# Optimization experiments

Measured on AMD Instinct MI355X. Metric: run time of the kernel, lower is better.

The kernel has to match this reference:

```python
import jax, jax.numpy as jnp
import numpy as np

B, S, HID, H = 2, 2048, 1024, 16
D_HEAD = HID // H  # 64
EPS = 1e-5


def _gammas():
    lo, hi = np.log(1.0 / 512.0), np.log(1.0 / 32.0)
    return (1.0 - np.exp(np.linspace(lo, hi, H))).astype(np.float32)


def _decay_mask():
    # D[h, n, m] = gamma_h^(n-m) for n >= m else 0  (causal exponential decay)
    gam = jnp.asarray(_gammas())                      # [H]
    pos = jnp.arange(S, dtype=jnp.float32)
    diff = pos[:, None] - pos[None, :]                # [S, S]
    keep = diff >= 0
    logg = jnp.log(gam)[:, None, None]                # [H,1,1]
    safe = jnp.where(keep, diff, 0.0)[None]           # avoid inf for masked entries
    return jnp.where(keep[None], jnp.exp(safe * logg), 0.0)  # [H, S, S]


def setup_inputs() -> dict:
    key = jax.random.key(0)
    ks = jax.random.split(key, 10)
    rn = lambda k, shape, s=1.0: jax.random.normal(k, shape, dtype=jnp.float32) * s
    return {
        "x": rn(ks[0], (B, S, HID)),
        "wq": rn(ks[1], (H, D_HEAD, D_HEAD), 1.0 / np.sqrt(D_HEAD)),
        "bq": rn(ks[2], (H, D_HEAD), 0.02),
        "wk": rn(ks[3], (H, D_HEAD, D_HEAD), 1.0 / np.sqrt(D_HEAD)),
        "bk": rn(ks[4], (H, D_HEAD), 0.02),
        "wv": rn(ks[5], (H, D_HEAD, D_HEAD), 1.0 / np.sqrt(D_HEAD)),
        "theta": rn(ks[6], (H, D_HEAD), 1.0 / D_HEAD),
        "gn_weight": jnp.ones((HID,), jnp.float32),
        "gn_bias": jnp.zeros((HID,), jnp.float32),
        "weight1": rn(ks[7], (HID, HID), 1.0 / HID),
        "weight2": rn(ks[8], (HID, HID), 1.0 / HID),
    }


def reference(x, wq, bq, wk, bk, wv, theta, gn_weight, gn_bias, weight1, weight2):
    # Per-head retention (all heads vectorized; torch loops over heads).
    xh = x.reshape(B, S, H, D_HEAD)
    q = jnp.einsum('bshd,hde->bshe', xh, wq) + bq
    k = jnp.einsum('bshd,hde->bshe', xh, wk) + bk
    v = jnp.einsum('bshd,hde->bshe', xh, wv)
    # Complex rotary factors exp(i*n*theta) on q, conj on k -> real part of q k^H:
    ang = jnp.arange(S, dtype=jnp.float32)[:, None, None] * theta[None]  # [S,H,d]
    cs, sn = jnp.cos(ang), jnp.sin(ang)
    scores = (jnp.einsum('bshd,bthd->bhst', q * cs, k * cs)
              + jnp.einsum('bshd,bthd->bhst', q * sn, k * sn))  # Re(QK^H) [B,H,S,S]
    scores = scores * _decay_mask()[None]                        # decay mask
    ret = jnp.einsum('bhst,bthd->bshd', scores, v)               # [B,S,H,d]
    # GroupNorm with groups = n_heads over channels (per-head normalization).
    mean = jnp.mean(ret, axis=-1, keepdims=True)
    var = jnp.var(ret, axis=-1, keepdims=True)
    retn = (ret - mean) * jax.lax.rsqrt(var + EPS)
    retn = retn.reshape(B, S, HID) * gn_weight + gn_bias
    # Swish gate on x @ W1, residual add, project with W2.
    gate = x @ weight1
    out = gate * jax.nn.sigmoid(gate) + retn
    return out @ weight2
```

## Files before the change

kernel.cpp:

```cpp
#include <hip/hip_runtime.h>
#include <cstdint>
#include <cstddef>

#define B_ 2
#define S_ 2048
#define HID_ 1024
#define H_ 16
#define DH_ 64

typedef __attribute__((ext_vector_type(8))) short short8;
typedef __attribute__((ext_vector_type(8))) unsigned short ushort8;
typedef __attribute__((ext_vector_type(4))) unsigned short ushort4v;
typedef __attribute__((ext_vector_type(4))) float floatx4;
typedef __attribute__((ext_vector_type(4))) float float4v;

static __device__ __forceinline__ unsigned short f2bf(float f) {
  unsigned int u = __float_as_uint(f);
  u += 0x7fffu + ((u >> 16) & 1u);
  return (unsigned short)(u >> 16);
}
static __device__ __forceinline__ float bf2f(unsigned short h) {
  return __uint_as_float(((unsigned int)h) << 16);
}

__global__ __launch_bounds__(256) void convert_kernel(
    const float* __restrict__ x, const float* __restrict__ w1,
    const float* __restrict__ w2, unsigned short* __restrict__ x_bf,
    unsigned short* __restrict__ w1t, unsigned short* __restrict__ w2t_hi,
    unsigned short* __restrict__ w2t_lo) {
  const int NX = B_ * S_ * HID_;
  const int NW = HID_ * HID_;
  int idx = blockIdx.x * 256 + threadIdx.x;
  if (idx < NX) {
    x_bf[idx] = f2bf(x[idx]);
  } else if (idx < NX + NW) {
    int i = idx - NX;
    int n = i >> 10, k = i & 1023;
    w1t[i] = f2bf(w1[k * HID_ + n]);
  } else if (idx < NX + 2 * NW) {
    int i = idx - NX - NW;
    int n = i >> 10, k = i & 1023;
    float v = w2[k * HID_ + n];
    unsigned short h = f2bf(v);
    w2t_hi[i] = h;
    w2t_lo[i] = f2bf(v - bf2f(h));
  }
}

__global__ __launch_bounds__(256) void qkv_kernel(
    const float* __restrict__ x, const float* __restrict__ wq,
    const float* __restrict__ bq, const float* __restrict__ wk,
    const float* __restrict__ bk, const float* __restrict__ wv,
    const float* __restrict__ theta,
    unsigned short* __restrict__ q_h, unsigned short* __restrict__ q_l,
    unsigned short* __restrict__ k_h, unsigned short* __restrict__ k_l,
    unsigned short* __restrict__ v_th, unsigned short* __restrict__ v_tl,
    int b) {
  __shared__ __align__(16) float xs[64 * 68];
  __shared__ __align__(16) float wqs[64 * 68];
  __shared__ __align__(16) float wks[64 * 68];
  __shared__ __align__(16) float wvs[64 * 68];

  int tid = threadIdx.x;
  int st = blockIdx.x, h = blockIdx.y;
  int s0 = st * 64;

#pragma unroll
  for (int i = 0; i < 4; ++i) {
    int cid = tid + i * 256;
    int r = cid >> 4, c4 = (cid & 15) * 4;
    *reinterpret_cast<float4v*>(&xs[r * 68 + c4]) =
        *reinterpret_cast<const float4v*>(x + ((size_t)(b * S_ + s0 + r)) * HID_ + h * DH_ + c4);
  }
#pragma unroll
  for (int i = 0; i < 4; ++i) {
    int cid = tid + i * 256;
    int d = cid >> 4, c4 = (cid & 15) * 4;
    *reinterpret_cast<float4v*>(&wqs[d * 68 + c4]) =
        *reinterpret_cast<const float4v*>(wq + (size_t)(h * DH_ + d) * DH_ + c4);
    *reinterpret_cast<float4v*>(&wks[d * 68 + c4]) =
        *reinterpret_cast<const float4v*>(wk + (size_t)(h * DH_ + d) * DH_ + c4);
    *reinterpret_cast<float4v*>(&wvs[d * 68 + c4]) =
        *reinterpret_cast<const float4v*>(wv + (size_t)(h * DH_ + d) * DH_ + c4);
  }
  __syncthreads();

  int rg = tid >> 3;
  int cg = tid & 7;
  int r0 = rg * 2, c0 = cg * 8;

  float aq[2][8], ak[2][8], av[2][8];
#pragma unroll
  for (int i = 0; i < 2; ++i)
#pragma unroll
    for (int j = 0; j < 8; ++j) { aq[i][j] = 0.f; ak[i][j] = 0.f; av[i][j] = 0.f; }

  for (int d = 0; d < 64; ++d) {
    float x0 = xs[(r0 + 0) * 68 + d];
    float x1 = xs[(r0 + 1) * 68 + d];
#pragma unroll
    for (int j = 0; j < 8; ++j) {
      float wqv = wqs[d * 68 + c0 + j];
      float wkv = wks[d * 68 + c0 + j];
      float wvv = wvs[d * 68 + c0 + j];
      aq[0][j] += x0 * wqv; aq[1][j] += x1 * wqv;
      ak[0][j] += x0 * wkv; ak[1][j] += x1 * wkv;
      av[0][j] += x0 * wvv; av[1][j] += x1 * wvv;
    }
  }

  float thv[8], bqv[8], bkv[8];
#pragma unroll
  for (int j = 0; j < 8; ++j) {
    thv[j] = theta[h * DH_ + c0 + j];
    bqv[j] = bq[h * DH_ + c0 + j];
    bkv[j] = bk[h * DH_ + c0 + j];
  }

  __syncthreads();
  unsigned short* VtH = reinterpret_cast<unsigned short*>(xs);
  unsigned short* VtL = reinterpret_cast<unsigned short*>(wqs);

#pragma unroll
  for (int i = 0; i < 2; ++i) {
    int s = s0 + r0 + i;
    size_t qb = ((size_t)h * S_ + s) * 128;
    ushort8 qch, qcl, qsh, qsl, kch, kcl, ksh, ksl;
#pragma unroll
    for (int j = 0; j < 8; ++j) {
      float q = aq[i][j] + bqv[j];
      float k = ak[i][j] + bkv[j];
      float ang = (float)s * thv[j];
      float cs = cosf(ang), sn = sinf(ang);
      float qc = q * cs, qs = q * sn;
      unsigned short hq1 = f2bf(qc);
      qch[j] = hq1;
      qcl[j] = f2bf(qc - bf2f(hq1));
      unsigned short hq2 = f2bf(qs);
      qsh[j] = hq2;
      qsl[j] = f2bf(qs - bf2f(hq2));
      float kc = k * cs, ksn = k * sn;
      unsigned short h1 = f2bf(kc);
      kch[j] = h1;
      kcl[j] = f2bf(kc - bf2f(h1));
      unsigned short h2 = f2bf(ksn);
      ksh[j] = h2;
      ksl[j] = f2bf(ksn - bf2f(h2));
      float vv = av[i][j];
      unsigned short vh1 = f2bf(vv);
      VtH[(c0 + j) * 72 + (r0 + i)] = vh1;
      VtL[(c0 + j) * 72 + (r0 + i)] = f2bf(vv - bf2f(vh1));
    }
    *reinterpret_cast<ushort8*>(q_h + qb + c0) = qch;
    *reinterpret_cast<ushort8*>(q_h + qb + 64 + c0) = qsh;
    *reinterpret_cast<ushort8*>(q_l + qb + c0) = qcl;
    *reinterpret_cast<ushort8*>(q_l + qb + 64 + c0) = qsl;
    *reinterpret_cast<ushort8*>(k_h + qb + c0) = kch;
    *reinterpret_cast<ushort8*>(k_h + qb + 64 + c0) = ksh;
    *reinterpret_cast<ushort8*>(k_l + qb + c0) = kcl;
    *reinterpret_cast<ushort8*>(k_l + qb + 64 + c0) = ksl;
  }
  __syncthreads();
#pragma unroll
  for (int i = 0; i < 2; ++i) {
    int cid = tid + i * 256;
    int d = cid >> 3, t8 = (cid & 7) * 8;
    size_t gb = ((size_t)(h * 64 + d)) * S_ + s0 + t8;
    *reinterpret_cast<ushort8*>(v_th + gb) = *reinterpret_cast<const ushort8*>(&VtH[d * 72 + t8]);
    *reinterpret_cast<ushort8*>(v_tl + gb) = *reinterpret_cast<const ushort8*>(&VtL[d * 72 + t8]);
  }
}

#define SCOFF(row, colb)   ((row) * 256 + ((colb) ^ (((row) & 7) << 4)))

__global__ __launch_bounds__(256, 2) void retention_fold_kernel(
    const unsigned short* __restrict__ q_h, const unsigned short* __restrict__ q_l,
    const unsigned short* __restrict__ k_h, const unsigned short* __restrict__ k_l,
    const unsigned short* __restrict__ v_th, const unsigned short* __restrict__ v_tl,
    const float* __restrict__ gn_w, const float* __restrict__ gn_b,
    float* __restrict__ retn, int b) {
  __shared__ __align__(16) unsigned short Kh[64 * 128];
  __shared__ __align__(16) unsigned short Kl[64 * 128];
  __shared__ __align__(16) unsigned short Vh[64 * 64];
  __shared__ __align__(16) unsigned short Vl[64 * 64];
  __shared__ __align__(16) float Sc[64 * 64];
  __shared__ float gnred[64][8];

  char* KhB = (char*)Kh;
  char* KlB = (char*)Kl;
  char* VhB = (char*)Vh;
  char* VlB = (char*)Vl;
  char* ScB = (char*)Sc;

  int tid = threadIdx.x;
  int w = tid >> 6;
  int lane = tid & 63, ln = lane & 15, quad = lane >> 4;
  int f = blockIdx.x;
  int h = ((f & 7) << 1) | ((f >> 7) & 1);
  int qp = (f >> 3) & 15;
  int qt = (f & 256) ? (31 - qp) : qp;
  int s0 = qt * 64;
  int prow = quad * 4;

  const float lo_c = -6.2383246250395075f, hi_c = -3.4657359027997265f;
  float gam = 1.f - __expf(lo_c + (hi_c - lo_c) * ((float)h * (1.f / 15.f)));
  float logg = __logf(gam);

  float rowf[4], colf[4];
#pragma unroll
  for (int rr = 0; rr < 4; ++rr)
    rowf[rr] = __expf((float)(w * 16 + prow + rr) * logg);
#pragma unroll
  for (int ns = 0; ns < 4; ++ns)
    colf[ns] = __expf(-(float)(ns * 16 + ln) * logg);

  const unsigned short* khb = k_h + (size_t)h * S_ * 128;
  const unsigned short* klb = k_l + (size_t)h * S_ * 128;
  const unsigned short* vhb = v_th + (size_t)h * 64 * S_;
  const unsigned short* vlb = v_tl + (size_t)h * 64 * S_;

  int sQ = s0 + w * 16 + ln;
  const unsigned short* qhp = q_h + ((size_t)h * S_ + sQ) * 128 + quad * 8;
  const unsigned short* qlp = q_l + ((size_t)h * S_ + sQ) * 128 + quad * 8;
  short8 qfh[4], qfl[4];
#pragma unroll
  for (int c = 0; c < 4; ++c) {
    qfh[c] = *reinterpret_cast<const short8*>(qhp + c * 32);
    qfl[c] = *reinterpret_cast<const short8*>(qlp + c * 32);
  }

  floatx4 accO[4];
#pragma unroll
  for (int i = 0; i < 4; ++i) accO[i] = (floatx4){0.f, 0.f, 0.f, 0.f};

  ushort8 skh[4], skl[4], svh[2], svl[2];
#pragma unroll
  for (int i = 0; i < 4; ++i) {
    int cid = tid + i * 256;
    int r = cid >> 4, c8 = (cid & 15) * 8;
    skh[i] = *reinterpret_cast<const ushort8*>(khb + (size_t)r * 128 + c8);
    skl[i] = *reinterpret_cast<const ushort8*>(klb + (size_t)r * 128 + c8);
  }
#pragma unroll
  for (int i = 0; i < 2; ++i) {
    int cid = tid + i * 256;
    int d = cid >> 3, t8 = (cid & 7) * 8;
    svh[i] = *reinterpret_cast<const ushort8*>(vhb + (size_t)d * S_ + t8);
    svl[i] = *reinterpret_cast<const ushort8*>(vlb + (size_t)d * S_ + t8);
  }
#pragma unroll
  for (int i = 0; i < 4; ++i) {
    int cid = tid + i * 256;
    int r = cid >> 4, c8 = (cid & 15) * 8;
    int ko = r * 256 + (((cid & 15) * 16) ^ ((r & 7) << 4));
    *reinterpret_cast<ushort8*>(KhB + ko) = skh[i];
    *reinterpret_cast<ushort8*>(KlB + ko) = skl[i];
  }
#pragma unroll
  for (int i = 0; i < 2; ++i) {
    int cid = tid + i * 256;
    int d = cid >> 3, t8 = (cid & 7) * 8;
    int vo = d * 128 + (((cid & 7) * 16) ^ ((d & 7) << 4));
    *reinterpret_cast<ushort8*>(VhB + vo) = svh[i];
    *reinterpret_cast<ushort8*>(VlB + vo) = svl[i];
  }
  if (qt >= 1) {
#pragma unroll
    for (int i = 0; i < 4; ++i) {
      int cid = tid + i * 256;
      int r = cid >> 4, c8 = (cid & 15) * 8;
      skh[i] = *reinterpret_cast<const ushort8*>(khb + ((size_t)(64 + r)) * 128 + c8);
      skl[i] = *reinterpret_cast<const ushort8*>(klb + ((size_t)(64 + r)) * 128 + c8);
    }
#pragma unroll
    for (int i = 0; i < 2; ++i) {
      int cid = tid + i * 256;
      int d = cid >> 3, t8 = (cid & 7) * 8;
      svh[i] = *reinterpret_cast<const ushort8*>(vhb + (size_t)d * S_ + 64 + t8);
      svl[i] = *reinterpret_cast<const ushort8*>(vlb + (size_t)d * S_ + 64 + t8);
    }
  }
  __syncthreads();

  for (int kt = 0; kt <= qt; ++kt) {
    floatx4 accS[4];
#pragma unroll
    for (int ns = 0; ns < 4; ++ns) {
      floatx4 a = (floatx4){0.f, 0.f, 0.f, 0.f};
      int row = ns * 16 + ln;
#pragma unroll
      for (int ks = 0; ks < 4; ++ks) {
        int off = row * 256 + ((ks * 64 + quad * 16) ^ ((ln & 7) << 4));
        short8 kh = *reinterpret_cast<const short8*>(KhB + off);
        short8 kl = *reinterpret_cast<const short8*>(KlB + off);
        a = __builtin_amdgcn_mfma_f32_16x16x32_bf16(qfh[ks], kh, a, 0, 0, 0);
        a = __builtin_amdgcn_mfma_f32_16x16x32_bf16(qfl[ks], kh, a, 0, 0, 0);
        a = __builtin_amdgcn_mfma_f32_16x16x32_bf16(qfh[ks], kl, a, 0, 0, 0);
      }
      accS[ns] = a;
    }

    float tf = __expf((float)(64 * (qt - kt)) * logg);
    float trf[4];
#pragma unroll
    for (int rr = 0; rr < 4; ++rr) trf[rr] = tf * rowf[rr];
    if (kt < qt) {
#pragma unroll
      for (int ns = 0; ns < 4; ++ns) {
        int col = ns * 16 + ln;
#pragma unroll
        for (int rr = 0; rr < 4; ++rr) {
          int row = w * 16 + prow + rr;
          *reinterpret_cast<float*>(ScB + SCOFF(row, col * 4)) =
              accS[ns][rr] * trf[rr] * colf[ns];
        }
      }
    } else {
#pragma unroll
      for (int ns = 0; ns < 4; ++ns) {
        int col = ns * 16 + ln;
#pragma unroll
        for (int rr = 0; rr < 4; ++rr) {
          int row = w * 16 + prow + rr;
          float v = accS[ns][rr] * trf[rr] * colf[ns];
          *reinterpret_cast<float*>(ScB + SCOFF(row, col * 4)) =
              (row >= col) ? v : 0.f;
        }
      }
    }

#pragma unroll
    for (int ks = 0; ks < 2; ++ks) {
      int prw = w * 16 + ln;
      int cb = ks * 128 + quad * 32;
      float4v p0 = *reinterpret_cast<const float4v*>(ScB + SCOFF(prw, cb));
      float4v p1 = *reinterpret_cast<const float4v*>(ScB + SCOFF(prw, cb + 16));
      short8 ph, pl;
#pragma unroll
      for (int j = 0; j < 4; ++j) {
        unsigned short hh = f2bf(p0[j]);
        ph[j] = (short)hh;
        pl[j] = (short)f2bf(p0[j] - bf2f(hh));
        unsigned short hh2 = f2bf(p1[j]);
        ph[4 + j] = (short)hh2;
        pl[4 + j] = (short)f2bf(p1[j] - bf2f(hh2));
      }
#pragma unroll
      for (int ds = 0; ds < 4; ++ds) {
        int d = ds * 16 + ln;
        int voff = d * 128 + ((ks * 64 + quad * 16) ^ ((ln & 7) << 4));
        short8 vh = *reinterpret_cast<const short8*>(VhB + voff);
        short8 vl = *reinterpret_cast<const short8*>(VlB + voff);
        accO[ds] = __builtin_amdgcn_mfma_f32_16x16x32_bf16(ph, vh, accO[ds], 0, 0, 0);
        accO[ds] = __builtin_amdgcn_mfma_f32_16x16x32_bf16(pl, vh, accO[ds], 0, 0, 0);
        accO[ds] = __builtin_amdgcn_mfma_f32_16x16x32_bf16(ph, vl, accO[ds], 0, 0, 0);
      }
    }

    __syncthreads();
    if (kt < qt) {
#pragma unroll
      for (int i = 0; i < 4; ++i) {
        int cid = tid + i * 256;
        int r = cid >> 4, c8 = (cid & 15) * 8;
        int ko = r * 256 + (((cid & 15) * 16) ^ ((r & 7) << 4));
        *reinterpret_cast<ushort8*>(KhB + ko) = skh[i];
        *reinterpret_cast<ushort8*>(KlB + ko) = skl[i];
      }
#pragma unroll
      for (int i = 0; i < 2; ++i) {
        int cid = tid + i * 256;
        int d = cid >> 3, t8 = (cid & 7) * 8;
        int vo = d * 128 + (((cid & 7) * 16) ^ ((d & 7) << 4));
        *reinterpret_cast<ushort8*>(VhB + vo) = svh[i];
        *reinterpret_cast<ushort8*>(VlB + vo) = svl[i];
      }
      if (kt + 2 <= qt) {
        int t0n = (kt + 2) * 64;
#pragma unroll
        for (int i = 0; i < 4; ++i) {
          int cid = tid + i * 256;
          int r = cid >> 4, c8 = (cid & 15) * 8;
          skh[i] = *reinterpret_cast<const ushort8*>(khb + ((size_t)(t0n + r)) * 128 + c8);
          skl[i] = *reinterpret_cast<const ushort8*>(klb + ((size_t)(t0n + r)) * 128 + c8);
        }
#pragma unroll
        for (int i = 0; i < 2; ++i) {
          int cid = tid + i * 256;
          int d = cid >> 3, t8 = (cid & 7) * 8;
          svh[i] = *reinterpret_cast<const ushort8*>(vhb + (size_t)d * S_ + t0n + t8);
          svl[i] = *reinterpret_cast<const ushort8*>(vlb + (size_t)d * S_ + t0n + t8);
        }
      }
      __syncthreads();
    }
  }

#pragma unroll
  for (int ds = 0; ds < 4; ++ds) {
#pragma unroll
    for (int rr = 0; rr < 4; ++rr) {
      int row = w * 16 + quad * 4 + rr;
      *reinterpret_cast<float*>(ScB + SCOFF(row, (ds * 16 + ln) * 4)) = accO[ds][rr];
    }
  }

  int r2 = tid >> 2;
  int sub = tid & 3;
  float a16[16];
#pragma unroll
  for (int c = 0; c < 4; ++c) {
    float4v t = *reinterpret_cast<const float4v*>(ScB + SCOFF(r2, sub * 64 + c * 16));
#pragma unroll
    for (int j = 0; j < 4; ++j) a16[c * 4 + j] = t[j];
  }

  float psum = 0.f, psq = 0.f;
#pragma unroll
  for (int i = 0; i < 16; ++i) { psum += a16[i]; psq += a16[i] * a16[i]; }
  gnred[r2][sub] = psum;
  gnred[r2][4 + sub] = psq;
  float sum = gnred[r2][0] + gnred[r2][1] + gnred[r2][2] + gnred[r2][3];
  float sq = gnred[r2][4] + gnred[r2][5] + gnred[r2][6] + gnred[r2][7];
  float mean = sum * (1.f / 64.f);
  float var = sq * (1.f / 64.f) - mean * mean;
  float rstd = rsqrtf(var + 1e-5f);

  size_t obase = ((size_t)(b * S_ + s0 + r2)) * HID_ + h * DH_ + sub * 16;
#pragma unroll
  for (int i = 0; i < 16; ++i) {
    float gw = gn_w[h * DH_ + sub * 16 + i];
    float gb = gn_b[h * DH_ + sub * 16 + i];
    retn[obase + i] = (a16[i] - mean) * rstd * gw + gb;
  }
}

__global__ __launch_bounds__(256) void gemm_gate_kernel(
    const unsigned short* __restrict__ A, const unsigned short* __restrict__ Bt,
    const float* __restrict__ retn, unsigned short* __restrict__ pre_hi,
    unsigned short* __restrict__ pre_lo) {
  const int K = HID_;
  __shared__ __align__(16) unsigned short Al[128 * 56];
  __shared__ __align__(16) unsigned short Bl[128 * 56];

  int tid = threadIdx.x;
  int lane = tid & 63, ln = lane & 15, quad = lane >> 4;
  int w = tid >> 6, wm = w >> 1, wn = w & 1;
  int m0 = blockIdx.y * 128, n0 = blockIdx.x * 128;

  floatx4 acc[4][4];
#pragma unroll
  for (int i = 0; i < 4; ++i)
#pragma unroll
    for (int j = 0; j < 4; ++j) acc[i][j] = (floatx4){0.f, 0.f, 0.f, 0.f};

  for (int k0 = 0; k0 < K; k0 += 32) {
    __syncthreads();
#pragma unroll
    for (int i = 0; i < 2; ++i) {
      int cid = tid + i * 256;
      int r = cid >> 2, c8 = (cid & 3) * 8;
      *reinterpret_cast<ushort8*>(&Al[r * 56 + c8]) =
          *reinterpret_cast<const ushort8*>(A + (size_t)(m0 + r) * K + k0 + c8);
      *reinterpret_cast<ushort8*>(&Bl[r * 56 + c8]) =
          *reinterpret_cast<const ushort8*>(Bt + (size_t)(n0 + r) * K + k0 + c8);
    }
    __syncthreads();

    short8 af[4], bfr[4];
#pragma unroll
    for (int i = 0; i < 4; ++i) {
      af[i] = *reinterpret_cast<const short8*>(&Al[(wm * 64 + i * 16 + ln) * 56 + quad * 8]);
      bfr[i] = *reinterpret_cast<const short8*>(&Bl[(wn * 64 + i * 16 + ln) * 56 + quad * 8]);
    }
#pragma unroll
    for (int mi = 0; mi < 4; ++mi)
#pragma unroll
      for (int ni = 0; ni < 4; ++ni)
        acc[mi][ni] = __builtin_amdgcn_mfma_f32_16x16x32_bf16(af[mi], bfr[ni], acc[mi][ni], 0, 0, 0);
  }

#pragma unroll
  for (int mi = 0; mi < 4; ++mi) {
#pragma unroll
    for (int r = 0; r < 4; ++r) {
      int row = m0 + wm * 64 + mi * 16 + quad * 4 + r;
#pragma unroll
      for (int ni = 0; ni < 4; ++ni) {
        int col = n0 + wn * 64 + ni * 16 + ln;
        float g = acc[mi][ni][r];
        float val = g * (1.f / (1.f + __expf(-g))) + retn[(size_t)row * HID_ + col];
        unsigned short hh = f2bf(val);
        size_t oidx = (size_t)row * HID_ + col;
        pre_hi[oidx] = hh;
        pre_lo[oidx] = f2bf(val - bf2f(hh));
      }
    }
  }
}

__global__ __launch_bounds__(256) void gemm_out_kernel(
    const unsigned short* __restrict__ Ah, const unsigned short* __restrict__ Alo,
    const unsigned short* __restrict__ Bth, const unsigned short* __restrict__ Btlo,
    float* __restrict__ out_f) {
  const int K = HID_;
  __shared__ __align__(16) unsigned short AhS[128 * 56];
  __shared__ __align__(16) unsigned short AlS[128 * 56];
  __shared__ __align__(16) unsigned short BhS[128 * 56];
  __shared__ __align__(16) unsigned short BlS[128 * 56];

  int tid = threadIdx.x;
  int lane = tid & 63, ln = lane & 15, quad = lane >> 4;
  int w = tid >> 6, wm = w >> 1, wn = w & 1;
  int m0 = blockIdx.y * 128, n0 = blockIdx.x * 128;

  floatx4 acc[4][4];
#pragma unroll
  for (int i = 0; i < 4; ++i)
#pragma unroll
    for (int j = 0; j < 4; ++j) acc[i][j] = (floatx4){0.f, 0.f, 0.f, 0.f};

  for (int k0 = 0; k0 < K; k0 += 32) {
    __syncthreads();
#pragma unroll
    for (int i = 0; i < 2; ++i) {
      int cid = tid + i * 256;
      int r = cid >> 2, c8 = (cid & 3) * 8;
      size_t ga = (size_t)(m0 + r) * K + k0 + c8;
      size_t gb = (size_t)(n0 + r) * K + k0 + c8;
      *reinterpret_cast<ushort8*>(&AhS[r * 56 + c8]) = *reinterpret_cast<const ushort8*>(Ah + ga);
      *reinterpret_cast<ushort8*>(&AlS[r * 56 + c8]) = *reinterpret_cast<const ushort8*>(Alo + ga);
      *reinterpret_cast<ushort8*>(&BhS[r * 56 + c8]) = *reinterpret_cast<const ushort8*>(Bth + gb);
      *reinterpret_cast<ushort8*>(&BlS[r * 56 + c8]) = *reinterpret_cast<const ushort8*>(Btlo + gb);
    }
    __syncthreads();

    short8 afh[4], afl[4], bfh[4], bfl[4];
#pragma unroll
    for (int i = 0; i < 4; ++i) {
      int ao = (wm * 64 + i * 16 + ln) * 56 + quad * 8;
      int bo = (wn * 64 + i * 16 + ln) * 56 + quad * 8;
      afh[i] = *reinterpret_cast<const short8*>(&AhS[ao]);
      afl[i] = *reinterpret_cast<const short8*>(&AlS[ao]);
      bfh[i] = *reinterpret_cast<const short8*>(&BhS[bo]);
      bfl[i] = *reinterpret_cast<const short8*>(&BlS[bo]);
    }
#pragma unroll
    for (int mi = 0; mi < 4; ++mi)
#pragma unroll
      for (int ni = 0; ni < 4; ++ni) {
        floatx4 a = acc[mi][ni];
        a = __builtin_amdgcn_mfma_f32_16x16x32_bf16(afh[mi], bfh[ni], a, 0, 0, 0);
        a = __builtin_amdgcn_mfma_f32_16x16x32_bf16(afl[mi], bfh[ni], a, 0, 0, 0);
        a = __builtin_amdgcn_mfma_f32_16x16x32_bf16(afh[mi], bfl[ni], a, 0, 0, 0);
        acc[mi][ni] = a;
      }
  }

#pragma unroll
  for (int mi = 0; mi < 4; ++mi) {
#pragma unroll
    for (int r = 0; r < 4; ++r) {
      int row = m0 + wm * 64 + mi * 16 + quad * 4 + r;
#pragma unroll
      for (int ni = 0; ni < 4; ++ni) {
        int col = n0 + wn * 64 + ni * 16 + ln;
        out_f[(size_t)row * HID_ + col] = acc[mi][ni][r];
      }
    }
  }
}

extern "C" void kernel_launch(void* const* d_in, const int* in_sizes, int n_in,
                              void* d_out, int out_size, void* d_ws,
                              size_t ws_size, hipStream_t stream) {
  (void)in_sizes; (void)n_in; (void)out_size; (void)ws_size;
  const float* x = (const float*)d_in[0];
  const float* wq = (const float*)d_in[1];
  const float* bq = (const float*)d_in[2];
  const float* wk = (const float*)d_in[3];
  const float* bk = (const float*)d_in[4];
  const float* wv = (const float*)d_in[5];
  const float* theta = (const float*)d_in[6];
  const float* gn_w = (const float*)d_in[7];
  const float* gn_b = (const float*)d_in[8];
  const float* w1 = (const float*)d_in[9];
  const float* w2 = (const float*)d_in[10];

  const size_t MB = 1024 * 1024;
  char* ws = (char*)d_ws;
  unsigned short* x_bf   = (unsigned short*)(ws + 0 * MB);
  unsigned short* w1t    = (unsigned short*)(ws + 8 * MB);
  unsigned short* w2t_hi = (unsigned short*)(ws + 10 * MB);
  unsigned short* w2t_lo = (unsigned short*)(ws + 12 * MB);
  unsigned short* q_h    = (unsigned short*)(ws + 14 * MB);
  unsigned short* q_l    = (unsigned short*)(ws + 22 * MB);
  unsigned short* k_h    = (unsigned short*)(ws + 30 * MB);
  unsigned short* k_l    = (unsigned short*)(ws + 38 * MB);
  unsigned short* v_th   = (unsigned short*)(ws + 46 * MB);
  unsigned short* v_tl   = (unsigned short*)(ws + 50 * MB);
  float*          retn   = (float*)(ws + 54 * MB);
  unsigned short* pre_hi = (unsigned short*)(ws + 14 * MB);
  unsigned short* pre_lo = (unsigned short*)(ws + 22 * MB);
  float* out = (float*)d_out;

  convert_kernel<<<dim3(24576), 256, 0, stream>>>(x, w1, w2, x_bf, w1t, w2t_hi, w2t_lo);
  for (int b = 0; b < B_; ++b) {
    qkv_kernel<<<dim3(S_ / 64, H_), 256, 0, stream>>>(
        x, wq, bq, wk, bk, wv, theta, q_h, q_l, k_h, k_l, v_th, v_tl, b);
    retention_fold_kernel<<<dim3(512), 256, 0, stream>>>(
        q_h, q_l, k_h, k_l, v_th, v_tl, gn_w, gn_b, retn, b);
  }
  gemm_gate_kernel<<<dim3(HID_ / 128, (B_ * S_) / 128), 256, 0, stream>>>(
      x_bf, w1t, retn, pre_hi, pre_lo);
  gemm_out_kernel<<<dim3(HID_ / 128, (B_ * S_) / 128), 256, 0, stream>>>(
      pre_hi, pre_lo, w2t_hi, w2t_lo, out);
}
```

Measured before the change: 378.2 us.

## Split causal retention key range across two blocks and combine with GroupNorm kernel

Each (head, query-tile) work item is split into two blocks, each covering half of the causal key tiles. Heaviest query tiles are launched first, so 1024 smaller blocks replace 512 uneven ones and the per-block load is more balanced. The partial outputs are written to a global scratch buffer. A new combine kernel sums the two halves and applies GroupNorm. This adds global traffic for the partials and an extra launch per batch in exchange for shorter tail latency.

```diff
diff --git a/kernel.cpp b/kernel.cpp
--- a/kernel.cpp
+++ b/kernel.cpp
@@ -173,18 +173,16 @@
 
 #define SCOFF(row, colb)   ((row) * 256 + ((colb) ^ (((row) & 7) << 4)))
 
-__global__ __launch_bounds__(256, 2) void retention_fold_kernel(
+__global__ __launch_bounds__(256, 2) void retention_split_kernel(
     const unsigned short* __restrict__ q_h, const unsigned short* __restrict__ q_l,
     const unsigned short* __restrict__ k_h, const unsigned short* __restrict__ k_l,
     const unsigned short* __restrict__ v_th, const unsigned short* __restrict__ v_tl,
-    const float* __restrict__ gn_w, const float* __restrict__ gn_b,
-    float* __restrict__ retn, int b) {
+    float* __restrict__ partial) {
   __shared__ __align__(16) unsigned short Kh[64 * 128];
   __shared__ __align__(16) unsigned short Kl[64 * 128];
   __shared__ __align__(16) unsigned short Vh[64 * 64];
   __shared__ __align__(16) unsigned short Vl[64 * 64];
   __shared__ __align__(16) float Sc[64 * 64];
-  __shared__ float gnred[64][8];
 
   char* KhB = (char*)Kh;
   char* KlB = (char*)Kl;
@@ -196,11 +194,15 @@
   int w = tid >> 6;
   int lane = tid & 63, ln = lane & 15, quad = lane >> 4;
   int f = blockIdx.x;
-  int h = ((f & 7) << 1) | ((f >> 7) & 1);
-  int qp = (f >> 3) & 15;
-  int qt = (f & 256) ? (31 - qp) : qp;
+  int h = ((f & 7) << 1) | ((f >> 3) & 1);
+  int half = (f >> 4) & 1;
+  int qt = 31 - (f >> 5);
   int s0 = qt * 64;
   int prow = quad * 4;
+
+  int m = (qt + 2) >> 1;
+  int kt0 = half ? m : 0;
+  int kt1 = half ? (qt + 1) : m;
 
   const float lo_c = -6.2383246250395075f, hi_c = -3.4657359027997265f;
   float gam = 1.f - __expf(lo_c + (hi_c - lo_c) * ((float)h * (1.f / 15.f)));
@@ -234,24 +236,25 @@
   for (int i = 0; i < 4; ++i) accO[i] = (floatx4){0.f, 0.f, 0.f, 0.f};
 
   ushort8 skh[4], skl[4], svh[2], svl[2];
+  int t00 = kt0 * 64;
 #pragma unroll
   for (int i = 0; i < 4; ++i) {
     int cid = tid + i * 256;
     int r = cid >> 4, c8 = (cid & 15) * 8;
-    skh[i] = *reinterpret_cast<const ushort8*>(khb + (size_t)r * 128 + c8);
-    skl[i] = *reinterpret_cast<const ushort8*>(klb + (size_t)r * 128 + c8);
+    skh[i] = *reinterpret_cast<const ushort8*>(khb + ((size_t)(t00 + r)) * 128 + c8);
+    skl[i] = *reinterpret_cast<const ushort8*>(klb + ((size_t)(t00 + r)) * 128 + c8);
   }
 #pragma unroll
   for (int i = 0; i < 2; ++i) {
     int cid = tid + i * 256;
     int d = cid >> 3, t8 = (cid & 7) * 8;
-    svh[i] = *reinterpret_cast<const ushort8*>(vhb + (size_t)d * S_ + t8);
-    svl[i] = *reinterpret_cast<const ushort8*>(vlb + (size_t)d * S_ + t8);
+    svh[i] = *reinterpret_cast<const ushort8*>(vhb + (size_t)d * S_ + t00 + t8);
+    svl[i] = *reinterpret_cast<const ushort8*>(vlb + (size_t)d * S_ + t00 + t8);
   }
 #pragma unroll
   for (int i = 0; i < 4; ++i) {
     int cid = tid + i * 256;
-    int r = cid >> 4, c8 = (cid & 15) * 8;
+    int r = cid >> 4;
     int ko = r * 256 + (((cid & 15) * 16) ^ ((r & 7) << 4));
     *reinterpret_cast<ushort8*>(KhB + ko) = skh[i];
     *reinterpret_cast<ushort8*>(KlB + ko) = skl[i];
@@ -259,30 +262,31 @@
 #pragma unroll
   for (int i = 0; i < 2; ++i) {
     int cid = tid + i * 256;
-    int d = cid >> 3, t8 = (cid & 7) * 8;
+    int d = cid >> 3;
     int vo = d * 128 + (((cid & 7) * 16) ^ ((d & 7) << 4));
     *reinterpret_cast<ushort8*>(VhB + vo) = svh[i];
     *reinterpret_cast<ushort8*>(VlB + vo) = svl[i];
   }
-  if (qt >= 1) {
+  if (kt0 + 1 < kt1) {
+    int t01 = (kt0 + 1) * 64;
 #pragma unroll
     for (int i = 0; i < 4; ++i) {
       int cid = tid + i * 256;
       int r = cid >> 4, c8 = (cid & 15) * 8;
-      skh[i] = *reinterpret_cast<const ushort8*>(khb + ((size_t)(64 + r)) * 128 + c8);
-      skl[i] = *reinterpret_cast<const ushort8*>(klb + ((size_t)(64 + r)) * 128 + c8);
+      skh[i] = *reinterpret_cast<const ushort8*>(khb + ((size_t)(t01 + r)) * 128 + c8);
+      skl[i] = *reinterpret_cast<const ushort8*>(klb + ((size_t)(t01 + r)) * 128 + c8);
     }
 #pragma unroll
     for (int i = 0; i < 2; ++i) {
       int cid = tid + i * 256;
       int d = cid >> 3, t8 = (cid & 7) * 8;
-      svh[i] = *reinterpret_cast<const ushort8*>(vhb + (size_t)d * S_ + 64 + t8);
-      svl[i] = *reinterpret_cast<const ushort8*>(vlb + (size_t)d * S_ + 64 + t8);
+      svh[i] = *reinterpret_cast<const ushort8*>(vhb + (size_t)d * S_ + t01 + t8);
+      svl[i] = *reinterpret_cast<const ushort8*>(vlb + (size_t)d * S_ + t01 + t8);
     }
   }
   __syncthreads();
 
-  for (int kt = 0; kt <= qt; ++kt) {
+  for (int kt = kt0; kt < kt1; ++kt) {
     floatx4 accS[4];
 #pragma unroll
     for (int ns = 0; ns < 4; ++ns) {
@@ -358,11 +362,11 @@
     }
 
     __syncthreads();
-    if (kt < qt) {
+    if (kt + 1 < kt1) {
 #pragma unroll
       for (int i = 0; i < 4; ++i) {
         int cid = tid + i * 256;
-        int r = cid >> 4, c8 = (cid & 15) * 8;
+        int r = cid >> 4;
         int ko = r * 256 + (((cid & 15) * 16) ^ ((r & 7) << 4));
         *reinterpret_cast<ushort8*>(KhB + ko) = skh[i];
         *reinterpret_cast<ushort8*>(KlB + ko) = skl[i];
@@ -370,12 +374,12 @@
 #pragma unroll
       for (int i = 0; i < 2; ++i) {
         int cid = tid + i * 256;
-        int d = cid >> 3, t8 = (cid & 7) * 8;
+        int d = cid >> 3;
         int vo = d * 128 + (((cid & 7) * 16) ^ ((d & 7) << 4));
         *reinterpret_cast<ushort8*>(VhB + vo) = svh[i];
         *reinterpret_cast<ushort8*>(VlB + vo) = svl[i];
       }
-      if (kt + 2 <= qt) {
+      if (kt + 2 < kt1) {
         int t0n = (kt + 2) * 64;
 #pragma unroll
         for (int i = 0; i < 4; ++i) {
@@ -396,23 +400,35 @@
     }
   }
 
+  float* pout = partial + ((size_t)(((h * 32 + qt) << 1) + half)) * 4096;
 #pragma unroll
   for (int ds = 0; ds < 4; ++ds) {
 #pragma unroll
     for (int rr = 0; rr < 4; ++rr) {
-      int row = w * 16 + quad * 4 + rr;
-      *reinterpret_cast<float*>(ScB + SCOFF(row, (ds * 16 + ln) * 4)) = accO[ds][rr];
-    }
-  }
+      pout[(w * 16 + quad * 4 + rr) * 64 + ds * 16 + ln] = accO[ds][rr];
+    }
+  }
+}
+
+__global__ __launch_bounds__(256) void combine_gn_kernel(
+    const float* __restrict__ partial, const float* __restrict__ gn_w,
+    const float* __restrict__ gn_b, float* __restrict__ retn, int b) {
+  __shared__ float gnred[64][8];
+  int tid = threadIdx.x;
+  int qi = blockIdx.x;
+  int h = qi >> 5, qt = qi & 31;
+  const float* p0 = partial + (size_t)qi * 8192;
+  const float* p1 = p0 + 4096;
 
   int r2 = tid >> 2;
   int sub = tid & 3;
   float a16[16];
 #pragma unroll
   for (int c = 0; c < 4; ++c) {
-    float4v t = *reinterpret_cast<const float4v*>(ScB + SCOFF(r2, sub * 64 + c * 16));
-#pragma unroll
-    for (int j = 0; j < 4; ++j) a16[c * 4 + j] = t[j];
+    float4v va = *reinterpret_cast<const float4v*>(p0 + r2 * 64 + sub * 16 + c * 4);
+    float4v vb = *reinterpret_cast<const float4v*>(p1 + r2 * 64 + sub * 16 + c * 4);
+#pragma unroll
+    for (int j = 0; j < 4; ++j) a16[c * 4 + j] = va[j] + vb[j];
   }
 
   float psum = 0.f, psq = 0.f;
@@ -426,7 +442,7 @@
   float var = sq * (1.f / 64.f) - mean * mean;
   float rstd = rsqrtf(var + 1e-5f);
 
-  size_t obase = ((size_t)(b * S_ + s0 + r2)) * HID_ + h * DH_ + sub * 16;
+  size_t obase = ((size_t)(b * S_ + qt * 64 + r2)) * HID_ + h * DH_ + sub * 16;
 #pragma unroll
   for (int i = 0; i < 16; ++i) {
     float gw = gn_w[h * DH_ + sub * 16 + i];
@@ -600,6 +616,7 @@
   unsigned short* v_th   = (unsigned short*)(ws + 46 * MB);
   unsigned short* v_tl   = (unsigned short*)(ws + 50 * MB);
   float*          retn   = (float*)(ws + 54 * MB);
+  float*          partial= (float*)(ws + 70 * MB);
   unsigned short* pre_hi = (unsigned short*)(ws + 14 * MB);
   unsigned short* pre_lo = (unsigned short*)(ws + 22 * MB);
   float* out = (float*)d_out;
@@ -608,8 +625,10 @@
   for (int b = 0; b < B_; ++b) {
     qkv_kernel<<<dim3(S_ / 64, H_), 256, 0, stream>>>(
         x, wq, bq, wk, bk, wv, theta, q_h, q_l, k_h, k_l, v_th, v_tl, b);
-    retention_fold_kernel<<<dim3(512), 256, 0, stream>>>(
-        q_h, q_l, k_h, k_l, v_th, v_tl, gn_w, gn_b, retn, b);
+    retention_split_kernel<<<dim3(1024), 256, 0, stream>>>(
+        q_h, q_l, k_h, k_l, v_th, v_tl, partial);
+    combine_gn_kernel<<<dim3(512), 256, 0, stream>>>(
+        partial, gn_w, gn_b, retn, b);
   }
   gemm_gate_kernel<<<dim3(HID_ / 128, (B_ * S_) / 128), 256, 0, stream>>>(
       x_bf, w1t, retn, pre_hi, pre_lo);
```

Result: faster. 345.4 us (-8.7%).
